# Performance work log

Measured on AMD Instinct MI355X. Metric: run time of the kernel, lower is better.

The kernel has to match this reference:

```python
import jax, jax.numpy as jnp
import numpy as np

B, SQ, SK, H, NH = 2, 2048, 2048, 2048, 16
HD = H // NH  # 128
NEG = -1e9


def setup_inputs() -> dict:
    key = jax.random.key(0)
    ks = jax.random.split(key, 8)
    hidden_states = jax.random.normal(ks[0], (B, SQ, H), dtype=jnp.float32)
    # key already transposed/expanded for baddbmm: [B*nh, head_dim, key_len]
    k = jax.random.normal(ks[1], (B * NH, HD, SK), dtype=jnp.float32)
    v = jax.random.normal(ks[2], (B, NH, SK, HD), dtype=jnp.float32)
    # additive float causal mask [B, 1, Sq, Sk]
    causal = jnp.tril(jnp.ones((SQ, SK), dtype=bool))
    attention_mask = jnp.where(causal, 0.0, NEG).astype(jnp.float32)
    attention_mask = jnp.broadcast_to(attention_mask[None, None], (B, 1, SQ, SK))
    w_q = jax.random.normal(ks[3], (H, H), dtype=jnp.float32) * 0.02
    b_q = jnp.zeros((H,), dtype=jnp.float32)
    w_proj = jax.random.normal(ks[4], (H, H), dtype=jnp.float32) * 0.02
    b_proj = jnp.zeros((H,), dtype=jnp.float32)
    return {
        "hidden_states": hidden_states,
        "key": k,
        "value": v,
        "attention_mask": attention_mask,
        "w_q": w_q,
        "b_q": b_q,
        "w_proj": w_proj,
        "b_proj": b_proj,
    }


def reference(hidden_states, key, value, attention_mask, w_q, b_q, w_proj, b_proj):
    dtype = hidden_states.dtype
    scale = 1.0 / (HD ** 0.5)  # scale_attn_weights=True, attention_multiplier=None
    # q projection: [B, Sq, H] -> [B, nh, Sq, hd]
    q = hidden_states @ w_q.T + b_q
    q = q.reshape(B, SQ, NH, HD).transpose(0, 2, 1, 3)
    # key comes in as [B*nh, hd, Sk]
    k = key.reshape(B, NH, HD, SK)
    # scores = mask + scale * q @ k  (baddbmm with beta=1)
    scores = attention_mask + scale * jnp.einsum("bhqd,bhdk->bhqk", q, k)
    # softmax in fp32 (attention_softmax_in_fp32=True), cast back
    probs = jax.nn.softmax(scores.astype(jnp.float32), axis=-1).astype(dtype)
    # attn_pdrop=0 -> no dropout
    out = jnp.einsum("bhqk,bhkd->bhqd", probs, value)  # [B, nh, Sq, hd]
    out = out.transpose(0, 2, 1, 3).reshape(B, SQ, H)
    out = out @ w_proj.T + b_proj  # resid_pdrop=0 -> no dropout
    return out
```

## Files before the change

### kernel.cpp

```cpp
#include <hip/hip_runtime.h>
#include <hip/hip_bf16.h>

typedef __bf16 bf16;
typedef __bf16 bf16x4 __attribute__((ext_vector_type(4)));
typedef __bf16 bf16x8 __attribute__((ext_vector_type(8)));
typedef float  f32x4  __attribute__((ext_vector_type(4)));
typedef unsigned int u32;

#define B_   2
#define SQ_  2048
#define SK_  2048
#define H_   2048
#define NH_  16
#define HD_  128
#define BH_  (B_*NH_)

__device__ inline void gl_lds16(const bf16* g, bf16* l) {
  __builtin_amdgcn_global_load_lds(
      (const __attribute__((address_space(1))) u32*)(const void*)g,
      (__attribute__((address_space(3))) u32*)(void*)l,
      16, 0, 0);
}

__device__ inline float exp2_fast(float x) {
  float r; asm("v_exp_f32 %0, %1" : "=v"(r) : "v"(x)); return r;
}

__global__ __launch_bounds__(256) void cvt_f32_bf16(const float* __restrict__ in,
                                                    bf16* __restrict__ out, int n4) {
  int i = blockIdx.x * blockDim.x + threadIdx.x;
  int stride = gridDim.x * blockDim.x;
  for (; i < n4; i += stride) {
    float4 v = ((const float4*)in)[i];
    bf16x4 w; w[0] = (bf16)v.x; w[1] = (bf16)v.y; w[2] = (bf16)v.z; w[3] = (bf16)v.w;
    ((bf16x4*)out)[i] = w;
  }
}

__global__ __launch_bounds__(256) void transpose_cvt(const float* __restrict__ in,
                                                     bf16* __restrict__ out, int R, int C) {
  __shared__ float tile[64][65];
  const int bh = blockIdx.z;
  const int r0 = blockIdx.y * 64, c0 = blockIdx.x * 64;
  const float* src = in + (size_t)bh * R * C;
  bf16* dst = out + (size_t)bh * R * C;
  const int t = threadIdx.x;
  const int tx = t & 15, ty = t >> 4;
#pragma unroll
  for (int p = 0; p < 4; ++p) {
    int rr = ty + p * 16;
    float4 v = *(const float4*)&src[(size_t)(r0 + rr) * C + c0 + tx * 4];
    tile[rr][tx * 4 + 0] = v.x; tile[rr][tx * 4 + 1] = v.y;
    tile[rr][tx * 4 + 2] = v.z; tile[rr][tx * 4 + 3] = v.w;
  }
  __syncthreads();
#pragma unroll
  for (int p = 0; p < 4; ++p) {
    int cc = ty + p * 16;
    bf16x4 w;
#pragma unroll
    for (int i = 0; i < 4; ++i) w[i] = (bf16)tile[tx * 4 + i][cc];
    *(bf16x4*)&dst[(size_t)(c0 + cc) * R + r0 + tx * 4] = w;
  }
}

template <typename OutT>
__global__ __launch_bounds__(256) void gemm_bt(const bf16* __restrict__ A,
                                               const bf16* __restrict__ Bw,
                                               const float* __restrict__ bias,
                                               OutT* __restrict__ C,
                                               int M, int N, int K, float osc) {
  __shared__ bf16 Abuf[128 * 32];
  __shared__ bf16 Bbuf[128 * 32];
  const int nbn = N >> 7;
  int wg = blockIdx.x, nwg = gridDim.x;
  int swz = (nwg & 7) ? wg : ((wg & 7) * (nwg >> 3) + (wg >> 3));
  int bm = swz / nbn, bn = swz % nbn;
  const int t = threadIdx.x, lane = t & 63, wid = t >> 6;
  const int r = lane & 15, g = lane >> 4;
  const int wr = wid >> 1, wc = wid & 1;
  const size_t m0 = (size_t)bm * 128, n0 = (size_t)bn * 128;

  f32x4 acc[4][4];
#pragma unroll
  for (int m = 0; m < 4; ++m)
#pragma unroll
    for (int n = 0; n < 4; ++n) acc[m][n] = (f32x4){0.f, 0.f, 0.f, 0.f};

  for (int k0 = 0; k0 < K; k0 += 32) {
    __syncthreads();
#pragma unroll
    for (int p = 0; p < 2; ++p) {
      int c = p * 256 + t;
      int row = c >> 2, off = c & 3;
      gl_lds16(A + (m0 + row) * K + k0 + off * 8, &Abuf[(p * 256 + wid * 64) * 8]);
      gl_lds16(Bw + (n0 + row) * K + k0 + off * 8, &Bbuf[(p * 256 + wid * 64) * 8]);
    }
    __syncthreads();
    bf16x8 af[4], bfr[4];
#pragma unroll
    for (int m = 0; m < 4; ++m)
      af[m] = *(const bf16x8*)&Abuf[(wr * 64 + m * 16 + r) * 32 + g * 8];
#pragma unroll
    for (int n = 0; n < 4; ++n)
      bfr[n] = *(const bf16x8*)&Bbuf[(wc * 64 + n * 16 + r) * 32 + g * 8];
#pragma unroll
    for (int m = 0; m < 4; ++m)
#pragma unroll
      for (int n = 0; n < 4; ++n)
        acc[m][n] = __builtin_amdgcn_mfma_f32_16x16x32_bf16(af[m], bfr[n], acc[m][n], 0, 0, 0);
  }

  float bv[4];
#pragma unroll
  for (int n = 0; n < 4; ++n) bv[n] = bias[n0 + wc * 64 + n * 16 + r];
#pragma unroll
  for (int m = 0; m < 4; ++m)
#pragma unroll
    for (int n = 0; n < 4; ++n)
#pragma unroll
      for (int rr = 0; rr < 4; ++rr) {
        size_t row = m0 + wr * 64 + m * 16 + g * 4 + rr;
        size_t col = n0 + wc * 64 + n * 16 + r;
        C[row * N + col] = (OutT)((acc[m][n][rr] + bv[n]) * osc);
      }
}

__device__ __forceinline__ void softmax_prep(const f32x4 (&s)[4], bool diag,
                                             int r, int g, int qrow_base, int s_base,
                                             float (&mrun)[4], float (&lpart)[4],
                                             f32x4 (&acc)[8], bf16* pldsw,
                                             bf16x8 (&pa)[2]) {
  float sv[4][4];
#pragma unroll
  for (int sb = 0; sb < 4; ++sb)
#pragma unroll
    for (int rr = 0; rr < 4; ++rr) {
      float x = s[sb][rr];
      if (diag && (s_base + sb * 16 + r > qrow_base + g * 4 + rr)) x = -3.0e38f;
      sv[sb][rr] = x;
    }
  float pm[4];
  bool cond = true;
#pragma unroll
  for (int rr = 0; rr < 4; ++rr) {
    pm[rr] = fmaxf(fmaxf(sv[0][rr], sv[1][rr]), fmaxf(sv[2][rr], sv[3][rr]));
    cond = cond && (pm[rr] <= mrun[rr] + 10.0f);
  }
  if (!__all(cond ? 1 : 0)) {
    f32x4 corrv;
#pragma unroll
    for (int rr = 0; rr < 4; ++rr) {
      float mx = pm[rr];
#pragma unroll
      for (int d = 1; d < 16; d <<= 1) mx = fmaxf(mx, __shfl_xor(mx, d));
      float mnew = fmaxf(mrun[rr], mx);
      float corr = exp2_fast(mrun[rr] - mnew);
      mrun[rr] = mnew;
      lpart[rr] *= corr;
      corrv[rr] = corr;
    }
#pragma unroll
    for (int nb = 0; nb < 8; ++nb) acc[nb] *= corrv;
  }
#pragma unroll
  for (int sb = 0; sb < 4; ++sb)
#pragma unroll
    for (int rr = 0; rr < 4; ++rr) {
      float p = exp2_fast(sv[sb][rr] - mrun[rr]);
      lpart[rr] += p;
      pldsw[(g * 4 + rr) * 68 + sb * 16 + r] = (bf16)p;
    }
#pragma unroll
  for (int k2 = 0; k2 < 2; ++k2)
    pa[k2] = *(const bf16x8*)&pldsw[r * 68 + k2 * 32 + g * 8];
}

__global__ __launch_bounds__(256, 1) void flash_attn(const bf16* __restrict__ Q,
                                                     const bf16* __restrict__ Kt,
                                                     const bf16* __restrict__ Vt,
                                                     bf16* __restrict__ O) {
  __shared__ bf16 Klds[2][64 * 128];
  __shared__ bf16 Vlds[2][128 * 64];
  __shared__ bf16 Plds[4][2][16 * 68];

  const int id = blockIdx.x;
  const int pr = (id >> 3) & 7;
  const int bh = (id & 7) + 8 * (id >> 6);
  const int qtA = 15 - pr, qtB = pr;
  const int b = bh >> 4, h = bh & 15;
  const int t = threadIdx.x, lane = t & 63, wid = t >> 6;
  const int r = lane & 15, g = lane >> 4;

  const bf16* Kbase = Kt + (size_t)bh * SK_ * HD_;
  const bf16* Vbase = Vt + (size_t)bh * HD_ * SK_;

  size_t kSrc[4], vSrc[4];
#pragma unroll
  for (int p = 0; p < 4; ++p) {
    int c = p * 256 + t;
    { int row = c >> 4, off = c & 15, src = off ^ (row & 7);
      kSrc[p] = (size_t)row * HD_ + src * 8; }
    { int row = c >> 3, off = c & 7, src = off ^ (row & 7);
      vSrc[p] = (size_t)row * SK_ + src * 8; }
  }

  int cur = 0;
#pragma unroll 1
  for (int pass = 0; pass < 2; ++pass) {
    const int qt = pass ? qtB : qtA;
    const int nst = 2 * qt + 2;
    const int wb = qt * 128 + wid * 32;

    bf16x8 qf[2][4];
#pragma unroll
    for (int m = 0; m < 2; ++m) {
      const size_t qrow = ((size_t)(b * SQ_ + wb + m * 16 + r)) * H_ + (size_t)h * HD_;
#pragma unroll
      for (int kk = 0; kk < 4; ++kk)
        qf[m][kk] = *(const bf16x8*)&Q[qrow + kk * 32 + g * 8];
    }

    f32x4 acc[2][8];
    float mrun[2][4], lpart[2][4];
#pragma unroll
    for (int m = 0; m < 2; ++m) {
#pragma unroll
      for (int i = 0; i < 8; ++i) acc[m][i] = (f32x4){0.f, 0.f, 0.f, 0.f};
#pragma unroll
      for (int i = 0; i < 4; ++i) { mrun[m][i] = -3.0e38f; lpart[m][i] = 0.f; }
    }

#pragma unroll
    for (int p = 0; p < 4; ++p) {
      gl_lds16(Kbase + kSrc[p], &Klds[cur][(p * 256 + wid * 64) * 8]);
      gl_lds16(Vbase + vSrc[p], &Vlds[cur][(p * 256 + wid * 64) * 8]);
    }
    asm volatile("s_waitcnt vmcnt(0)" ::: "memory");
    __syncthreads();

#pragma unroll 1
    for (int st = 0; st < nst; ++st) {
      if (st + 1 < nst) {
        const size_t ks = (size_t)(st + 1) * 64 * HD_;
        const size_t vs = (size_t)(st + 1) * 64;
#pragma unroll
        for (int p = 0; p < 4; ++p) {
          gl_lds16(Kbase + ks + kSrc[p], &Klds[cur ^ 1][(p * 256 + wid * 64) * 8]);
          gl_lds16(Vbase + vs + vSrc[p], &Vlds[cur ^ 1][(p * 256 + wid * 64) * 8]);
        }
      }
      const int sb0 = st * 64;
      const bool act1 = (sb0 <= wb + 31);
      const bool act0 = (sb0 <= wb + 15);

      if (act1) {
        f32x4 sA[2][4];
#pragma unroll
        for (int m = 0; m < 2; ++m)
#pragma unroll
          for (int sb = 0; sb < 4; ++sb) sA[m][sb] = (f32x4){0.f, 0.f, 0.f, 0.f};
        __builtin_amdgcn_s_setprio(1);
        if (act0) {
#pragma unroll
          for (int sb = 0; sb < 4; ++sb) {
            const int srow = sb * 16 + r;
#pragma unroll
            for (int kk = 0; kk < 4; ++kk) {
              bf16x8 kf = *(const bf16x8*)&Klds[cur][srow * 128 + (((kk * 4 + g) ^ (srow & 7)) * 8)];
              sA[0][sb] = __builtin_amdgcn_mfma_f32_16x16x32_bf16(qf[0][kk], kf, sA[0][sb], 0, 0, 0);
              sA[1][sb] = __builtin_amdgcn_mfma_f32_16x16x32_bf16(qf[1][kk], kf, sA[1][sb], 0, 0, 0);
            }
          }
        } else {
#pragma unroll
          for (int sb = 0; sb < 4; ++sb) {
            const int srow = sb * 16 + r;
#pragma unroll
            for (int kk = 0; kk < 4; ++kk) {
              bf16x8 kf = *(const bf16x8*)&Klds[cur][srow * 128 + (((kk * 4 + g) ^ (srow & 7)) * 8)];
              sA[1][sb] = __builtin_amdgcn_mfma_f32_16x16x32_bf16(qf[1][kk], kf, sA[1][sb], 0, 0, 0);
            }
          }
        }
        __builtin_amdgcn_s_setprio(0);

        bf16x8 paf[2][2];
        if (act0)
          softmax_prep(sA[0], sb0 + 63 > wb, r, g, wb, sb0,
                       mrun[0], lpart[0], acc[0], &Plds[wid][0][0], paf[0]);
        softmax_prep(sA[1], sb0 + 63 > wb + 16, r, g, wb + 16, sb0,
                     mrun[1], lpart[1], acc[1], &Plds[wid][1][0], paf[1]);

        __builtin_amdgcn_s_setprio(1);
        if (act0) {
#pragma unroll
          for (int nb = 0; nb < 8; ++nb) {
            const int drow = nb * 16 + r;
#pragma unroll
            for (int k2 = 0; k2 < 2; ++k2) {
              bf16x8 vf = *(const bf16x8*)&Vlds[cur][drow * 64 + (((k2 * 4 + g) ^ (drow & 7)) * 8)];
              acc[0][nb] = __builtin_amdgcn_mfma_f32_16x16x32_bf16(paf[0][k2], vf, acc[0][nb], 0, 0, 0);
              acc[1][nb] = __builtin_amdgcn_mfma_f32_16x16x32_bf16(paf[1][k2], vf, acc[1][nb], 0, 0, 0);
            }
          }
        } else {
#pragma unroll
          for (int nb = 0; nb < 8; ++nb) {
            const int drow = nb * 16 + r;
#pragma unroll
            for (int k2 = 0; k2 < 2; ++k2) {
              bf16x8 vf = *(const bf16x8*)&Vlds[cur][drow * 64 + (((k2 * 4 + g) ^ (drow & 7)) * 8)];
              acc[1][nb] = __builtin_amdgcn_mfma_f32_16x16x32_bf16(paf[1][k2], vf, acc[1][nb], 0, 0, 0);
            }
          }
        }
        __builtin_amdgcn_s_setprio(0);
      }

      asm volatile("s_waitcnt vmcnt(0)" ::: "memory");
      __syncthreads();
      cur ^= 1;
    }

#pragma unroll
    for (int m = 0; m < 2; ++m) {
      float inv[4];
#pragma unroll
      for (int rr = 0; rr < 4; ++rr) {
        float la = lpart[m][rr];
#pragma unroll
        for (int d = 1; d < 16; d <<= 1) la += __shfl_xor(la, d);
        inv[rr] = 1.0f / la;
      }
#pragma unroll
      for (int nb = 0; nb < 8; ++nb)
#pragma unroll
        for (int rr = 0; rr < 4; ++rr) {
          size_t row = (size_t)(b * SQ_ + wb + m * 16 + g * 4 + rr);
          O[row * H_ + (size_t)h * HD_ + nb * 16 + r] = (bf16)(acc[m][nb][rr] * inv[rr]);
        }
    }
  }
}

extern "C" void kernel_launch(void* const* d_in, const int* in_sizes, int n_in,
                              void* d_out, int out_size, void* d_ws, size_t ws_size,
                              hipStream_t stream) {
  const float* hidden = (const float*)d_in[0];
  const float* key    = (const float*)d_in[1];
  const float* value  = (const float*)d_in[2];
  const float* w_q    = (const float*)d_in[4];
  const float* b_q    = (const float*)d_in[5];
  const float* w_proj = (const float*)d_in[6];
  const float* b_proj = (const float*)d_in[7];
  float* out = (float*)d_out;

  const size_t N_HID = (size_t)B_ * SQ_ * H_;
  const size_t N_W   = (size_t)H_ * H_;
  const size_t N_KV  = (size_t)BH_ * SK_ * HD_;
  const float SC2 = 0.08838834764831845f * 1.4426950408889634f;

  bf16* hid_bf  = (bf16*)d_ws;
  bf16* wq_bf   = hid_bf + N_HID;
  bf16* wp_bf   = wq_bf + N_W;
  bf16* k_bf    = wp_bf + N_W;
  bf16* vt_bf   = k_bf + N_KV;
  bf16* q_bf    = vt_bf + N_KV;
  bf16* attn_bf = hid_bf;

  cvt_f32_bf16<<<2048, 256, 0, stream>>>(hidden, hid_bf, (int)(N_HID / 4));
  cvt_f32_bf16<<<1024, 256, 0, stream>>>(w_q, wq_bf, (int)(N_W / 4));
  cvt_f32_bf16<<<1024, 256, 0, stream>>>(w_proj, wp_bf, (int)(N_W / 4));
  transpose_cvt<<<dim3(SK_ / 64, HD_ / 64, BH_), 256, 0, stream>>>(key, k_bf, HD_, SK_);
  transpose_cvt<<<dim3(HD_ / 64, SK_ / 64, BH_), 256, 0, stream>>>(value, vt_bf, SK_, HD_);

  gemm_bt<bf16><<<(B_ * SQ_ / 128) * (H_ / 128), 256, 0, stream>>>(
      hid_bf, wq_bf, b_q, q_bf, B_ * SQ_, H_, H_, SC2);

  flash_attn<<<256, 256, 0, stream>>>(q_bf, k_bf, vt_bf, attn_bf);

  gemm_bt<float><<<(B_ * SQ_ / 128) * (H_ / 128), 256, 0, stream>>>(
      attn_bf, wp_bf, b_proj, out, B_ * SQ_, H_, H_, 1.0f);
}
```

Before: 249.0 us.

## Split long causal attention rows across two blocks with merge kernel, fuse prep launches

The flash attention grid is doubled to 512 blocks. The long q-tile of each pair is split along the key dimension into two halves. One half stores unnormalized partial outputs plus max/sum stats, and a new merge kernel combines them. The other block finishes the short tile, which aims to balance work and double occupancy (launch bounds 2). The three fp32-to-bf16 conversions and the two transposes are also fused into single launches to cut launch overhead. The cost is an extra kernel plus partial-buffer traffic, and bf16 rounding of the partial accumulators.

```diff
diff --git a/kernel.cpp b/kernel.cpp
--- a/kernel.cpp
+++ b/kernel.cpp
@@ -26,10 +26,16 @@
   float r; asm("v_exp_f32 %0, %1" : "=v"(r) : "v"(x)); return r;
 }
 
-__global__ __launch_bounds__(256) void cvt_f32_bf16(const float* __restrict__ in,
-                                                    bf16* __restrict__ out, int n4) {
-  int i = blockIdx.x * blockDim.x + threadIdx.x;
-  int stride = gridDim.x * blockDim.x;
+__global__ __launch_bounds__(256) void cvt3_f32_bf16(const float* __restrict__ a, bf16* __restrict__ ao,
+                                                     const float* __restrict__ b, bf16* __restrict__ bo,
+                                                     const float* __restrict__ c, bf16* __restrict__ co) {
+  const int blk = blockIdx.x;
+  const float* in; bf16* out; int n4, bstart, nblk;
+  if (blk < 1024)      { in = a; out = ao; n4 = (B_ * SQ_ * H_) / 4; bstart = 0;    nblk = 1024; }
+  else if (blk < 1536) { in = b; out = bo; n4 = (H_ * H_) / 4;       bstart = 1024; nblk = 512; }
+  else                 { in = c; out = co; n4 = (H_ * H_) / 4;       bstart = 1536; nblk = 512; }
+  int i = (blk - bstart) * 256 + threadIdx.x;
+  const int stride = nblk * 256;
   for (; i < n4; i += stride) {
     float4 v = ((const float4*)in)[i];
     bf16x4 w; w[0] = (bf16)v.x; w[1] = (bf16)v.y; w[2] = (bf16)v.z; w[3] = (bf16)v.w;
@@ -37,13 +43,23 @@
   }
 }
 
-__global__ __launch_bounds__(256) void transpose_cvt(const float* __restrict__ in,
-                                                     bf16* __restrict__ out, int R, int C) {
+__global__ __launch_bounds__(256) void transpose_cvt2(const float* __restrict__ key,
+                                                      const float* __restrict__ value,
+                                                      bf16* __restrict__ kout,
+                                                      bf16* __restrict__ vout) {
   __shared__ float tile[64][65];
-  const int bh = blockIdx.z;
-  const int r0 = blockIdx.y * 64, c0 = blockIdx.x * 64;
-  const float* src = in + (size_t)bh * R * C;
-  bf16* dst = out + (size_t)bh * R * C;
+  const int id = blockIdx.x;
+  const float* src; bf16* dst; int R, C, r0, c0, bh;
+  if (id < 2048) {
+    src = key; dst = kout; R = HD_; C = SK_;
+    c0 = (id & 31) * 64; r0 = ((id >> 5) & 1) * 64; bh = id >> 6;
+  } else {
+    const int j = id - 2048;
+    src = value; dst = vout; R = SK_; C = HD_;
+    c0 = (j & 1) * 64; r0 = ((j >> 1) & 31) * 64; bh = j >> 6;
+  }
+  src += (size_t)bh * R * C;
+  dst += (size_t)bh * R * C;
   const int t = threadIdx.x;
   const int tx = t & 15, ty = t >> 4;
 #pragma unroll
@@ -176,40 +192,48 @@
     pa[k2] = *(const bf16x8*)&pldsw[r * 68 + k2 * 32 + g * 8];
 }
 
-__global__ __launch_bounds__(256, 1) void flash_attn(const bf16* __restrict__ Q,
+__global__ __launch_bounds__(256, 2) void flash_attn(const bf16* __restrict__ Q,
                                                      const bf16* __restrict__ Kt,
                                                      const bf16* __restrict__ Vt,
-                                                     bf16* __restrict__ O) {
+                                                     bf16* __restrict__ O,
+                                                     bf16* __restrict__ part,
+                                                     float2* __restrict__ mlbuf) {
   __shared__ bf16 Klds[2][64 * 128];
   __shared__ bf16 Vlds[2][128 * 64];
-  __shared__ bf16 Plds[4][2][16 * 68];
+  __shared__ bf16 Plds[4][16 * 68];
 
   const int id = blockIdx.x;
   const int pr = (id >> 3) & 7;
-  const int bh = (id & 7) + 8 * (id >> 6);
+  const int hf = (id >> 6) & 1;
+  const int bh = (id & 7) + 8 * (id >> 7);
   const int qtA = 15 - pr, qtB = pr;
+  const int nA = 2 * qtA + 2, nB = 2 * qtB + 2;
   const int b = bh >> 4, h = bh & 15;
   const int t = threadIdx.x, lane = t & 63, wid = t >> 6;
   const int r = lane & 15, g = lane >> 4;
 
   const bf16* Kbase = Kt + (size_t)bh * SK_ * HD_;
   const bf16* Vbase = Vt + (size_t)bh * HD_ * SK_;
-
-  size_t kSrc[4], vSrc[4];
+  bf16* pldsw = &Plds[wid][0];
+
+  u32 kSrc[4], vSrc[4];
 #pragma unroll
   for (int p = 0; p < 4; ++p) {
     int c = p * 256 + t;
     { int row = c >> 4, off = c & 15, src = off ^ (row & 7);
-      kSrc[p] = (size_t)row * HD_ + src * 8; }
+      kSrc[p] = (u32)(row * HD_ + src * 8); }
     { int row = c >> 3, off = c & 7, src = off ^ (row & 7);
-      vSrc[p] = (size_t)row * SK_ + src * 8; }
+      vSrc[p] = (u32)(row * SK_ + src * 8); }
   }
 
   int cur = 0;
+  const int npass = hf ? 2 : 1;
 #pragma unroll 1
-  for (int pass = 0; pass < 2; ++pass) {
-    const int qt = pass ? qtB : qtA;
-    const int nst = 2 * qt + 2;
+  for (int ps = 0; ps < npass; ++ps) {
+    int qt, lo, hi, partial;
+    if (!hf)          { qt = qtA; lo = 0;  hi = 17; partial = 1; }
+    else if (ps == 0) { qt = qtA; lo = 17; hi = nA; partial = 1; }
+    else              { qt = qtB; lo = 0;  hi = nB; partial = 0; }
     const int wb = qt * 128 + wid * 32;
 
     bf16x8 qf[2][4];
@@ -231,28 +255,30 @@
       for (int i = 0; i < 4; ++i) { mrun[m][i] = -3.0e38f; lpart[m][i] = 0.f; }
     }
 
-#pragma unroll
-    for (int p = 0; p < 4; ++p) {
-      gl_lds16(Kbase + kSrc[p], &Klds[cur][(p * 256 + wid * 64) * 8]);
-      gl_lds16(Vbase + vSrc[p], &Vlds[cur][(p * 256 + wid * 64) * 8]);
+    {
+      const size_t ks = (size_t)lo * (64 * HD_), vs = (size_t)lo * 64;
+#pragma unroll
+      for (int p = 0; p < 4; ++p) {
+        gl_lds16(Kbase + ks + kSrc[p], &Klds[cur][(p * 256 + wid * 64) * 8]);
+        gl_lds16(Vbase + vs + vSrc[p], &Vlds[cur][(p * 256 + wid * 64) * 8]);
+      }
     }
     asm volatile("s_waitcnt vmcnt(0)" ::: "memory");
     __syncthreads();
 
 #pragma unroll 1
-    for (int st = 0; st < nst; ++st) {
-      if (st + 1 < nst) {
-        const size_t ks = (size_t)(st + 1) * 64 * HD_;
-        const size_t vs = (size_t)(st + 1) * 64;
+    for (int st = lo; st < hi; ++st) {
+      if (st + 1 < hi) {
+        const size_t ks = (size_t)(st + 1) * (64 * HD_), vs = (size_t)(st + 1) * 64;
 #pragma unroll
         for (int p = 0; p < 4; ++p) {
           gl_lds16(Kbase + ks + kSrc[p], &Klds[cur ^ 1][(p * 256 + wid * 64) * 8]);
           gl_lds16(Vbase + vs + vSrc[p], &Vlds[cur ^ 1][(p * 256 + wid * 64) * 8]);
         }
       }
-      const int sb0 = st * 64;
-      const bool act1 = (sb0 <= wb + 31);
-      const bool act0 = (sb0 <= wb + 15);
+      const int s0 = st * 64;
+      const bool act1 = (s0 <= wb + 31);
+      const bool act0 = (s0 <= wb + 15);
 
       if (act1) {
         f32x4 sA[2][4];
@@ -287,10 +313,10 @@
 
         bf16x8 paf[2][2];
         if (act0)
-          softmax_prep(sA[0], sb0 + 63 > wb, r, g, wb, sb0,
-                       mrun[0], lpart[0], acc[0], &Plds[wid][0][0], paf[0]);
-        softmax_prep(sA[1], sb0 + 63 > wb + 16, r, g, wb + 16, sb0,
-                     mrun[1], lpart[1], acc[1], &Plds[wid][1][0], paf[1]);
+          softmax_prep(sA[0], s0 + 63 > wb, r, g, wb, s0,
+                       mrun[0], lpart[0], acc[0], pldsw, paf[0]);
+        softmax_prep(sA[1], s0 + 63 > wb + 16, r, g, wb + 16, s0,
+                     mrun[1], lpart[1], acc[1], pldsw, paf[1]);
 
         __builtin_amdgcn_s_setprio(1);
         if (act0) {
@@ -323,25 +349,79 @@
       cur ^= 1;
     }
 
-#pragma unroll
-    for (int m = 0; m < 2; ++m) {
-      float inv[4];
-#pragma unroll
-      for (int rr = 0; rr < 4; ++rr) {
-        float la = lpart[m][rr];
-#pragma unroll
-        for (int d = 1; d < 16; d <<= 1) la += __shfl_xor(la, d);
-        inv[rr] = 1.0f / la;
-      }
-#pragma unroll
-      for (int nb = 0; nb < 8; ++nb)
+    if (partial) {
+      const int slot = (hf * 8 + pr) * 32 + bh;
+      bf16* pbase = part + (size_t)slot * (128 * 128);
+#pragma unroll
+      for (int m = 0; m < 2; ++m) {
+        float lred[4];
 #pragma unroll
         for (int rr = 0; rr < 4; ++rr) {
-          size_t row = (size_t)(b * SQ_ + wb + m * 16 + g * 4 + rr);
-          O[row * H_ + (size_t)h * HD_ + nb * 16 + r] = (bf16)(acc[m][nb][rr] * inv[rr]);
-        }
-    }
-  }
+          float la = lpart[m][rr];
+#pragma unroll
+          for (int d = 1; d < 16; d <<= 1) la += __shfl_xor(la, d);
+          lred[rr] = la;
+        }
+#pragma unroll
+        for (int nb = 0; nb < 8; ++nb)
+#pragma unroll
+          for (int rr = 0; rr < 4; ++rr) {
+            int row = wid * 32 + m * 16 + g * 4 + rr;
+            pbase[row * 128 + nb * 16 + r] = (bf16)acc[m][nb][rr];
+          }
+        if (r == 0) {
+#pragma unroll
+          for (int rr = 0; rr < 4; ++rr) {
+            int row = wid * 32 + m * 16 + g * 4 + rr;
+            mlbuf[(size_t)slot * 128 + row] = float2{mrun[m][rr], lred[rr]};
+          }
+        }
+      }
+    } else {
+#pragma unroll
+      for (int m = 0; m < 2; ++m) {
+        float inv[4];
+#pragma unroll
+        for (int rr = 0; rr < 4; ++rr) {
+          float la = lpart[m][rr];
+#pragma unroll
+          for (int d = 1; d < 16; d <<= 1) la += __shfl_xor(la, d);
+          inv[rr] = 1.0f / la;
+        }
+#pragma unroll
+        for (int nb = 0; nb < 8; ++nb)
+#pragma unroll
+          for (int rr = 0; rr < 4; ++rr) {
+            size_t row = (size_t)(b * SQ_ + wb + m * 16 + g * 4 + rr);
+            O[row * H_ + (size_t)h * HD_ + nb * 16 + r] = (bf16)(acc[m][nb][rr] * inv[rr]);
+          }
+      }
+    }
+  }
+}
+
+__global__ __launch_bounds__(256) void flash_merge(const bf16* __restrict__ part,
+                                                   const float2* __restrict__ mlbuf,
+                                                   bf16* __restrict__ O) {
+  const int idx = blockIdx.x * 2 + (threadIdx.x >> 7);
+  const int d = threadIdx.x & 127;
+  const int row = idx & 127;
+  const int bh = (idx >> 7) & 31;
+  const int pr = idx >> 12;
+  const int qtA = 15 - pr;
+  const int b = bh >> 4, h = bh & 15;
+  const int slot0 = pr * 32 + bh;
+  const int slot1 = (8 + pr) * 32 + bh;
+  const float2 ml0 = mlbuf[(size_t)slot0 * 128 + row];
+  const float2 ml1 = mlbuf[(size_t)slot1 * 128 + row];
+  const float M = fmaxf(ml0.x, ml1.x);
+  const float c0 = exp2_fast(ml0.x - M);
+  const float c1 = exp2_fast(ml1.x - M);
+  const float inv = 1.0f / (c0 * ml0.y + c1 * ml1.y);
+  const float a0 = (float)part[(size_t)slot0 * (128 * 128) + row * 128 + d];
+  const float a1 = (float)part[(size_t)slot1 * (128 * 128) + row * 128 + d];
+  const size_t orow = (size_t)(b * SQ_ + qtA * 128 + row);
+  O[orow * H_ + (size_t)h * HD_ + d] = (bf16)((c0 * a0 + c1 * a1) * inv);
 }
 
 extern "C" void kernel_launch(void* const* d_in, const int* in_sizes, int n_in,
@@ -367,18 +447,18 @@
   bf16* k_bf    = wp_bf + N_W;
   bf16* vt_bf   = k_bf + N_KV;
   bf16* q_bf    = vt_bf + N_KV;
+  bf16* part_bf = q_bf + N_HID;
+  float2* ml_bf = (float2*)(part_bf + (size_t)512 * 128 * 128);
   bf16* attn_bf = hid_bf;
 
-  cvt_f32_bf16<<<2048, 256, 0, stream>>>(hidden, hid_bf, (int)(N_HID / 4));
-  cvt_f32_bf16<<<1024, 256, 0, stream>>>(w_q, wq_bf, (int)(N_W / 4));
-  cvt_f32_bf16<<<1024, 256, 0, stream>>>(w_proj, wp_bf, (int)(N_W / 4));
-  transpose_cvt<<<dim3(SK_ / 64, HD_ / 64, BH_), 256, 0, stream>>>(key, k_bf, HD_, SK_);
-  transpose_cvt<<<dim3(HD_ / 64, SK_ / 64, BH_), 256, 0, stream>>>(value, vt_bf, SK_, HD_);
+  cvt3_f32_bf16<<<2048, 256, 0, stream>>>(hidden, hid_bf, w_q, wq_bf, w_proj, wp_bf);
+  transpose_cvt2<<<4096, 256, 0, stream>>>(key, value, k_bf, vt_bf);
 
   gemm_bt<bf16><<<(B_ * SQ_ / 128) * (H_ / 128), 256, 0, stream>>>(
       hid_bf, wq_bf, b_q, q_bf, B_ * SQ_, H_, H_, SC2);
 
-  flash_attn<<<256, 256, 0, stream>>>(q_bf, k_bf, vt_bf, attn_bf);
+  flash_attn<<<512, 256, 0, stream>>>(q_bf, k_bf, vt_bf, attn_bf, part_bf, ml_bf);
+  flash_merge<<<16384, 256, 0, stream>>>(part_bf, ml_bf, attn_bf);
 
   gemm_bt<float><<<(B_ * SQ_ / 128) * (H_ / 128), 256, 0, stream>>>(
       attn_bf, wp_bf, b_proj, out, B_ * SQ_, H_, H_, 1.0f);
```

New measurement: 224.9 us. 1.11x faster.
